# Kernel optimization log

Measured on AMD Instinct MI355X. Metric: run time of the kernel, lower is better.

Reference implementation:

```python
import jax, jax.numpy as jnp
import numpy as np

N, E = 50000, 640000
D_IN, D_OUT, N_BASES = 128, 128, 8


def setup_inputs() -> dict:
    key = jax.random.key(0)
    k1, k2, k3, k4, k5, k6 = jax.random.split(key, 6)
    x = jax.random.normal(k1, (N, D_IN), dtype=jnp.float32)
    edge_index = jax.random.randint(k2, (2, E), 0, N, dtype=jnp.int64)
    # basis-decomposed relation weights (num_relations=1)
    bases = jax.random.normal(k3, (N_BASES, D_IN, D_OUT), dtype=jnp.float32) * 0.05
    comp = jax.random.normal(k4, (1, N_BASES), dtype=jnp.float32)
    root = jax.random.normal(k5, (D_IN, D_OUT), dtype=jnp.float32) * 0.05
    bias = jax.random.normal(k6, (D_OUT,), dtype=jnp.float32) * 0.01
    return {"x": x, "edge_index": edge_index, "bases": bases,
            "comp": comp, "root": root, "bias": bias}


def reference(x, edge_index, bases, comp, root, bias):
    # W[rel=0] = sum_b comp[0,b] * bases[b]  -> [D_IN, D_OUT]
    W = jnp.einsum('b,bio->io', comp[0], bases)
    src = edge_index[0]  # message sources (x_j)
    dst = edge_index[1]  # aggregation targets
    # gather -> scatter-add (aggr='add'), then relation-specific transform
    agg = jax.ops.segment_sum(x[src], dst, num_segments=x.shape[0])  # [N, D_IN]
    out = agg @ W + x @ root + bias  # root/self-loop transform + bias
    return out
```

## Files before the change

### kernel.cpp

```cpp
#include <hip/hip_runtime.h>

#define N_NODES 50000
#define N_EDGES 640000
#define D 128
#define NB 8
#define PAD 32
#define NSTRIP 3125
#define GRID_G 1024

typedef _Float16 half_t;
typedef __attribute__((ext_vector_type(8))) _Float16 half8;
typedef __attribute__((ext_vector_type(4))) float f32x4;

__global__ __launch_bounds__(256)
void init_kernel(const float* __restrict__ bases,
                 const float* __restrict__ comp,
                 const float* __restrict__ root,
                 half_t* __restrict__ Wt,
                 half_t* __restrict__ Rt,
                 int* __restrict__ cnt) {
    int i = blockIdx.x * 256 + threadIdx.x;
    if (i < N_NODES) cnt[i] = 0;
    if (i < D * D) {
        int ii = i >> 7, o = i & 127;
        float acc = 0.f;
#pragma unroll
        for (int b = 0; b < NB; ++b)
            acc += comp[b] * bases[((size_t)b * D + ii) * D + o];
        Wt[o * D + ii] = (half_t)acc;
        Rt[o * D + ii] = (half_t)root[i];
    }
}

__global__ __launch_bounds__(256, 4)
void gemm_kernel(const float* __restrict__ x,
                 const half_t* __restrict__ Wt,
                 const half_t* __restrict__ Rt,
                 const float* __restrict__ bias,
                 half_t* __restrict__ y,
                 float* __restrict__ out) {
    const int tid  = threadIdx.x;
    const int wave = tid >> 6;
    const int lane = tid & 63;
    const int m    = lane & 15;
    const int quad = lane >> 4;
    const int gw   = blockIdx.x * 4 + wave;
    const int q    = gw & 3;
    const int s0   = gw >> 2;
    const int SSTR = GRID_G;

    half8 bw[2][4], br[2][4];
    float bb[2];
#pragma unroll
    for (int t = 0; t < 2; ++t) {
        const int nt = 2 * q + t;
        const half_t* wp = Wt + (nt * 16 + m) * D + quad * 8;
        const half_t* rp = Rt + (nt * 16 + m) * D + quad * 8;
#pragma unroll
        for (int kk = 0; kk < 4; ++kk) {
            bw[t][kk] = *(const half8*)(wp + kk * 32);
            br[t][kk] = *(const half8*)(rp + kk * 32);
        }
        bb[t] = bias[nt * 16 + m];
    }

    const float4* x4 = (const float4*)x;
    for (int s = s0; s < NSTRIP; s += SSTR) {
        size_t ab = (size_t)(s * 16 + m) * 32 + quad * 2;
        half8 a[4];
#pragma unroll
        for (int kk = 0; kk < 4; ++kk) {
            float4 v0 = x4[ab + kk * 8];
            float4 v1 = x4[ab + kk * 8 + 1];
            half8 h;
            h[0] = (half_t)v0.x; h[1] = (half_t)v0.y; h[2] = (half_t)v0.z; h[3] = (half_t)v0.w;
            h[4] = (half_t)v1.x; h[5] = (half_t)v1.y; h[6] = (half_t)v1.z; h[7] = (half_t)v1.w;
            a[kk] = h;
        }

        f32x4 accW[2], accR[2];
#pragma unroll
        for (int t = 0; t < 2; ++t) {
            accW[t] = (f32x4){0.f, 0.f, 0.f, 0.f};
            accR[t] = (f32x4){0.f, 0.f, 0.f, 0.f};
        }
#pragma unroll
        for (int t = 0; t < 2; ++t)
#pragma unroll
            for (int kk = 0; kk < 4; ++kk) {
                accW[t] = __builtin_amdgcn_mfma_f32_16x16x32_f16(a[kk], bw[t][kk], accW[t], 0, 0, 0);
                accR[t] = __builtin_amdgcn_mfma_f32_16x16x32_f16(a[kk], br[t][kk], accR[t], 0, 0, 0);
            }

#pragma unroll
        for (int t = 0; t < 2; ++t) {
            int col = (2 * q + t) * 16 + m;
#pragma unroll
            for (int r = 0; r < 4; ++r) {
                int row = s * 16 + quad * 4 + r;
                y[(size_t)row * D + col]   = (half_t)accW[t][r];
                out[(size_t)row * D + col] = accR[t][r] + bb[t];
            }
        }
    }
}

__global__ __launch_bounds__(256)
void bucket_kernel(const int* __restrict__ eidx,
                   const half_t* __restrict__ y,
                   float* __restrict__ out,
                   int* __restrict__ cnt,
                   int* __restrict__ bucket) {
    int e = blockIdx.x * 256 + threadIdx.x;
    if (e >= N_EDGES) return;
    int src = eidx[e];
    int dst = eidx[N_EDGES + e];
    int pos = atomicAdd(&cnt[dst], 1);
    if (pos < PAD) {
        bucket[(size_t)dst * PAD + pos] = src;
    } else {
        const half_t* yr = y + (size_t)src * D;
        float* op = out + (size_t)dst * D;
        for (int q = 0; q < D; ++q) atomicAdd(op + q, (float)yr[q]);
    }
}

__global__ __launch_bounds__(256)
void gather_kernel(const int* __restrict__ cnt,
                   const int* __restrict__ bucket,
                   const half_t* __restrict__ y,
                   float* __restrict__ out) {
    int node = blockIdx.x * 16 + (threadIdx.x >> 4);
    int q = threadIdx.x & 15;
    if (node >= N_NODES) return;
    int c = cnt[node];
    if (c > PAD) c = PAD;
    const int* b = bucket + (size_t)node * PAD;
    float acc[8] = {0.f, 0.f, 0.f, 0.f, 0.f, 0.f, 0.f, 0.f};
    int i = 0;
    for (; i + 8 <= c; i += 8) {
        int4 s0 = *(const int4*)(b + i);
        int4 s1 = *(const int4*)(b + i + 4);
        half8 v0 = *(const half8*)(y + (size_t)s0.x * D + q * 8);
        half8 v1 = *(const half8*)(y + (size_t)s0.y * D + q * 8);
        half8 v2 = *(const half8*)(y + (size_t)s0.z * D + q * 8);
        half8 v3 = *(const half8*)(y + (size_t)s0.w * D + q * 8);
        half8 v4 = *(const half8*)(y + (size_t)s1.x * D + q * 8);
        half8 v5 = *(const half8*)(y + (size_t)s1.y * D + q * 8);
        half8 v6 = *(const half8*)(y + (size_t)s1.z * D + q * 8);
        half8 v7 = *(const half8*)(y + (size_t)s1.w * D + q * 8);
#pragma unroll
        for (int j = 0; j < 8; ++j)
            acc[j] += ((float)v0[j] + (float)v1[j]) + ((float)v2[j] + (float)v3[j])
                    + ((float)v4[j] + (float)v5[j]) + ((float)v6[j] + (float)v7[j]);
    }
    for (; i + 4 <= c; i += 4) {
        int4 s = *(const int4*)(b + i);
        half8 v0 = *(const half8*)(y + (size_t)s.x * D + q * 8);
        half8 v1 = *(const half8*)(y + (size_t)s.y * D + q * 8);
        half8 v2 = *(const half8*)(y + (size_t)s.z * D + q * 8);
        half8 v3 = *(const half8*)(y + (size_t)s.w * D + q * 8);
#pragma unroll
        for (int j = 0; j < 8; ++j)
            acc[j] += ((float)v0[j] + (float)v1[j]) + ((float)v2[j] + (float)v3[j]);
    }
    for (; i < c; ++i) {
        half8 v = *(const half8*)(y + (size_t)b[i] * D + q * 8);
#pragma unroll
        for (int j = 0; j < 8; ++j) acc[j] += (float)v[j];
    }
    float4* op = (float4*)(out + (size_t)node * D + q * 8);
    float4 o0 = op[0], o1 = op[1];
    o0.x += acc[0]; o0.y += acc[1]; o0.z += acc[2]; o0.w += acc[3];
    o1.x += acc[4]; o1.y += acc[5]; o1.z += acc[6]; o1.w += acc[7];
    op[0] = o0; op[1] = o1;
}

extern "C" void kernel_launch(void* const* d_in, const int* in_sizes, int n_in,
                              void* d_out, int out_size, void* d_ws, size_t ws_size,
                              hipStream_t stream) {
    const float* x     = (const float*)d_in[0];
    const int*   eidx  = (const int*)d_in[1];
    const float* bases = (const float*)d_in[2];
    const float* comp  = (const float*)d_in[3];
    const float* root  = (const float*)d_in[4];
    const float* bias  = (const float*)d_in[5];
    float* out = (float*)d_out;

    char* ws = (char*)d_ws;
    half_t* y      = (half_t*)ws;
    half_t* Wt     = (half_t*)(ws + 12800000);
    half_t* Rt     = (half_t*)(ws + 12832768);
    int*    cnt    = (int*)   (ws + 12865536);
    int*    bucket = (int*)   (ws + 13065536);

    init_kernel<<<(N_NODES + 255) / 256, 256, 0, stream>>>(
        bases, comp, root, Wt, Rt, cnt);
    gemm_kernel<<<GRID_G, 256, 0, stream>>>(
        x, Wt, Rt, bias, y, out);
    bucket_kernel<<<(N_EDGES + 255) / 256, 256, 0, stream>>>(
        eidx, y, out, cnt, bucket);
    gather_kernel<<<(N_NODES + 15) / 16, 256, 0, stream>>>(
        cnt, bucket, y, out);
}
```

Baseline: 167.9 us.

## Bin edge buckets by source chunk and store 16-bit source indices

Each destination's bucket is split into 8 sub-buckets keyed by which 6250-node source range the edge comes from, with a counter per (dst, chunk) cell. Source indices are stored as u16. The gather kernel walks the chunks in order. The intent is to group y-row reads by source range for better cache locality and to shrink the index footprint, at the cost of an 8x larger counter array, more padded bucket space, and short per-chunk loops that mostly take the scalar tail.

```diff
diff --git a/kernel.cpp b/kernel.cpp
--- a/kernel.cpp
+++ b/kernel.cpp
@@ -4,13 +4,16 @@
 #define N_EDGES 640000
 #define D 128
 #define NB 8
-#define PAD 32
+#define CH 8
+#define CSZ 6250
+#define PADC 12
 #define NSTRIP 3125
 #define GRID_G 1024
 
 typedef _Float16 half_t;
 typedef __attribute__((ext_vector_type(8))) _Float16 half8;
 typedef __attribute__((ext_vector_type(4))) float f32x4;
+typedef unsigned short u16;
 
 __global__ __launch_bounds__(256)
 void init_kernel(const float* __restrict__ bases,
@@ -20,7 +23,7 @@
                  half_t* __restrict__ Rt,
                  int* __restrict__ cnt) {
     int i = blockIdx.x * 256 + threadIdx.x;
-    if (i < N_NODES) cnt[i] = 0;
+    if (i < N_NODES * CH) cnt[i] = 0;
     if (i < D * D) {
         int ii = i >> 7, o = i & 127;
         float acc = 0.f;
@@ -47,7 +50,6 @@
     const int gw   = blockIdx.x * 4 + wave;
     const int q    = gw & 3;
     const int s0   = gw >> 2;
-    const int SSTR = GRID_G;
 
     half8 bw[2][4], br[2][4];
     float bb[2];
@@ -65,7 +67,7 @@
     }
 
     const float4* x4 = (const float4*)x;
-    for (int s = s0; s < NSTRIP; s += SSTR) {
+    for (int s = s0; s < NSTRIP; s += GRID_G) {
         size_t ab = (size_t)(s * 16 + m) * 32 + quad * 2;
         half8 a[4];
 #pragma unroll
@@ -110,14 +112,16 @@
                    const half_t* __restrict__ y,
                    float* __restrict__ out,
                    int* __restrict__ cnt,
-                   int* __restrict__ bucket) {
+                   u16* __restrict__ bucket) {
     int e = blockIdx.x * 256 + threadIdx.x;
     if (e >= N_EDGES) return;
     int src = eidx[e];
     int dst = eidx[N_EDGES + e];
-    int pos = atomicAdd(&cnt[dst], 1);
-    if (pos < PAD) {
-        bucket[(size_t)dst * PAD + pos] = src;
+    int ch  = src / CSZ;
+    int cell = dst * CH + ch;
+    int pos = atomicAdd(&cnt[cell], 1);
+    if (pos < PADC) {
+        bucket[(size_t)cell * PADC + pos] = (u16)src;
     } else {
         const half_t* yr = y + (size_t)src * D;
         float* op = out + (size_t)dst * D;
@@ -127,48 +131,43 @@
 
 __global__ __launch_bounds__(256)
 void gather_kernel(const int* __restrict__ cnt,
-                   const int* __restrict__ bucket,
+                   const u16* __restrict__ bucket,
                    const half_t* __restrict__ y,
                    float* __restrict__ out) {
     int node = blockIdx.x * 16 + (threadIdx.x >> 4);
     int q = threadIdx.x & 15;
     if (node >= N_NODES) return;
-    int c = cnt[node];
-    if (c > PAD) c = PAD;
-    const int* b = bucket + (size_t)node * PAD;
+
+    const int4* cp = (const int4*)(cnt + node * CH);
+    int4 ca = cp[0], cb = cp[1];
+    int cArr[8] = {ca.x, ca.y, ca.z, ca.w, cb.x, cb.y, cb.z, cb.w};
+    const u16* nb = bucket + (size_t)node * CH * PADC;
+
     float acc[8] = {0.f, 0.f, 0.f, 0.f, 0.f, 0.f, 0.f, 0.f};
-    int i = 0;
-    for (; i + 8 <= c; i += 8) {
-        int4 s0 = *(const int4*)(b + i);
-        int4 s1 = *(const int4*)(b + i + 4);
-        half8 v0 = *(const half8*)(y + (size_t)s0.x * D + q * 8);
-        half8 v1 = *(const half8*)(y + (size_t)s0.y * D + q * 8);
-        half8 v2 = *(const half8*)(y + (size_t)s0.z * D + q * 8);
-        half8 v3 = *(const half8*)(y + (size_t)s0.w * D + q * 8);
-        half8 v4 = *(const half8*)(y + (size_t)s1.x * D + q * 8);
-        half8 v5 = *(const half8*)(y + (size_t)s1.y * D + q * 8);
-        half8 v6 = *(const half8*)(y + (size_t)s1.z * D + q * 8);
-        half8 v7 = *(const half8*)(y + (size_t)s1.w * D + q * 8);
-#pragma unroll
-        for (int j = 0; j < 8; ++j)
-            acc[j] += ((float)v0[j] + (float)v1[j]) + ((float)v2[j] + (float)v3[j])
-                    + ((float)v4[j] + (float)v5[j]) + ((float)v6[j] + (float)v7[j]);
-    }
-    for (; i + 4 <= c; i += 4) {
-        int4 s = *(const int4*)(b + i);
-        half8 v0 = *(const half8*)(y + (size_t)s.x * D + q * 8);
-        half8 v1 = *(const half8*)(y + (size_t)s.y * D + q * 8);
-        half8 v2 = *(const half8*)(y + (size_t)s.z * D + q * 8);
-        half8 v3 = *(const half8*)(y + (size_t)s.w * D + q * 8);
-#pragma unroll
-        for (int j = 0; j < 8; ++j)
-            acc[j] += ((float)v0[j] + (float)v1[j]) + ((float)v2[j] + (float)v3[j]);
-    }
-    for (; i < c; ++i) {
-        half8 v = *(const half8*)(y + (size_t)b[i] * D + q * 8);
-#pragma unroll
-        for (int j = 0; j < 8; ++j) acc[j] += (float)v[j];
-    }
+#pragma unroll
+    for (int ch = 0; ch < CH; ++ch) {
+        int c = cArr[ch];
+        if (c > PADC) c = PADC;
+        const u16* b = nb + ch * PADC;
+        int i = 0;
+        for (; i + 4 <= c; i += 4) {
+            int s0 = b[i], s1 = b[i + 1], s2 = b[i + 2], s3 = b[i + 3];
+            half8 v0 = *(const half8*)(y + (size_t)s0 * D + q * 8);
+            half8 v1 = *(const half8*)(y + (size_t)s1 * D + q * 8);
+            half8 v2 = *(const half8*)(y + (size_t)s2 * D + q * 8);
+            half8 v3 = *(const half8*)(y + (size_t)s3 * D + q * 8);
+#pragma unroll
+            for (int j = 0; j < 8; ++j)
+                acc[j] += ((float)v0[j] + (float)v1[j]) + ((float)v2[j] + (float)v3[j]);
+        }
+        for (; i < c; ++i) {
+            int s = b[i];
+            half8 v = *(const half8*)(y + (size_t)s * D + q * 8);
+#pragma unroll
+            for (int j = 0; j < 8; ++j) acc[j] += (float)v[j];
+        }
+    }
+
     float4* op = (float4*)(out + (size_t)node * D + q * 8);
     float4 o0 = op[0], o1 = op[1];
     o0.x += acc[0]; o0.y += acc[1]; o0.z += acc[2]; o0.w += acc[3];
@@ -192,9 +191,9 @@
     half_t* Wt     = (half_t*)(ws + 12800000);
     half_t* Rt     = (half_t*)(ws + 12832768);
     int*    cnt    = (int*)   (ws + 12865536);
-    int*    bucket = (int*)   (ws + 13065536);
-
-    init_kernel<<<(N_NODES + 255) / 256, 256, 0, stream>>>(
+    u16*    bucket = (u16*)   (ws + 14465536);
+
+    init_kernel<<<(N_NODES * CH + 255) / 256, 256, 0, stream>>>(
         bases, comp, root, Wt, Rt, cnt);
     gemm_kernel<<<GRID_G, 256, 0, stream>>>(
         x, Wt, Rt, bias, y, out);
```

Result: slower. 185.9 us (+10.7%).
